# Kernel optimization log

Hardware: AMD Instinct MI355X
Metric: run time of the kernel (lower is better)

Reference implementation:

```python
import jax, jax.numpy as jnp
import numpy as np

N_NODES = 50000
N_EDGES = 640000
HID = 128
EDGE_FEAT = 4
NUM_G = 20
R_MIN, R_MAX = 0.0, 10.0

def setup_inputs() -> dict:
    key = jax.random.key(0)
    ks = jax.random.split(key, 16)
    s = lambda d: 1.0 / np.sqrt(d)
    return {
        'h': jax.random.normal(ks[0], (N_NODES, HID), jnp.float32),
        'x': jax.random.normal(ks[1], (N_NODES, 3), jnp.float32),
        'edge_index': jax.random.randint(ks[2], (2, N_EDGES), 0, N_NODES, dtype=jnp.int64),
        'mask_ligand': jnp.ones((N_NODES,), jnp.float32),
        'edge_attr': jax.random.normal(ks[3], (N_EDGES, EDGE_FEAT), jnp.float32),
        'We1': jax.random.normal(ks[4], (2*HID+EDGE_FEAT+NUM_G, HID), jnp.float32) * s(2*HID+EDGE_FEAT+NUM_G),
        'be1': jnp.zeros((HID,), jnp.float32),
        'We2': jax.random.normal(ks[5], (HID, HID), jnp.float32) * s(HID),
        'be2': jnp.zeros((HID,), jnp.float32),
        'Winf': jax.random.normal(ks[6], (HID, 1), jnp.float32) * s(HID),
        'binf': jnp.zeros((1,), jnp.float32),
        'Wx1': jax.random.normal(ks[7], (HID, HID), jnp.float32) * s(HID),
        'bx1': jnp.zeros((HID,), jnp.float32),
        'Wx2': jax.random.normal(ks[8], (HID, 1), jnp.float32) * 0.001 * s(HID),
        'Wn1': jax.random.normal(ks[9], (2*HID, HID), jnp.float32) * s(2*HID),
        'bn1': jnp.zeros((HID,), jnp.float32),
        'Wn2': jax.random.normal(ks[10], (HID, HID), jnp.float32) * s(HID),
        'bn2': jnp.zeros((HID,), jnp.float32),
    }

def reference(h, x, edge_index, mask_ligand, edge_attr,
              We1, be1, We2, be2, Winf, binf, Wx1, bx1, Wx2, Wn1, bn1, Wn2, bn2):
    n = h.shape[0]
    src, dst = edge_index[0], edge_index[1]
    hi, hj = h[dst], h[src]                      # [E, H] gathers
    rel_x = x[dst] - x[src]                      # [E, 3]
    d_sq = jnp.sum(rel_x**2, axis=-1, keepdims=True)  # [E, 1]
    d = jnp.sqrt(d_sq + 1e-8)
    # GaussianSmearing(r_min=0, r_max=10, num_gaussians=20)
    offset = jnp.linspace(R_MIN, R_MAX, NUM_G, dtype=h.dtype)
    coeff = -0.5 / (offset[1] - offset[0])**2
    d_feat = jnp.exp(coeff * (d - offset)**2)    # [E, 20]
    edge_feat = jnp.concatenate([d_feat, edge_attr], axis=-1)
    # edge MLP (2 layers, silu, act_last=True)
    z = jnp.concatenate([hi, hj, edge_feat], axis=-1)
    mij = jax.nn.silu(jax.nn.silu(z @ We1 + be1) @ We2 + be2)  # [E, H]
    eij = jax.nn.sigmoid(mij @ Winf + binf)      # [E, 1]
    mi = jax.ops.segment_sum(mij * eij, dst, num_segments=n)   # [N, H]
    # node MLP (2 layers, silu, no act on last)
    nz = jnp.concatenate([mi, h], axis=-1)
    h_out = h + (jax.nn.silu(nz @ Wn1 + bn1) @ Wn2 + bn2)
    # coordinate update
    xg = jnp.tanh(jax.nn.silu(mij @ Wx1 + bx1) @ Wx2)          # [E, 1]
    delta_x = jax.ops.segment_sum(rel_x / (d + 1.0) * xg, dst, num_segments=n)
    x_out = x + delta_x * mask_ligand[:, None]
    return h_out, x_out
```

## Files before the change

kernel.cpp:

```cpp
#include <hip/hip_runtime.h>
#include <math.h>

#define NN 50000
#define NE 640000
#define H 128
#define EPB 32
#define NPB 32
#define ZB 296
#define BB 136
#define KP1 288
#define NZB 264

typedef __attribute__((ext_vector_type(8))) unsigned short u16x8;
typedef __attribute__((ext_vector_type(8))) __bf16 bf16x8;
typedef __attribute__((ext_vector_type(2))) __bf16 bf16x2;
typedef __attribute__((ext_vector_type(4))) float f32x4;

__device__ __forceinline__ float silu_f(float v) {
    return v / (1.0f + __expf(-v));
}

__device__ __forceinline__ unsigned short f2bf(float f) {
    unsigned int u = __builtin_bit_cast(unsigned int, f);
    u += 0x7FFFu + ((u >> 16) & 1u);
    return (unsigned short)(u >> 16);
}

__device__ __forceinline__ float bf2f(unsigned short s) {
    unsigned int u = ((unsigned int)s) << 16;
    return __builtin_bit_cast(float, u);
}

__device__ __forceinline__ unsigned int pkbf(float lo, float hi) {
#if __has_builtin(__builtin_amdgcn_cvt_pk_bf16_f32)
    bf16x2 v = __builtin_amdgcn_cvt_pk_bf16_f32(lo, hi);
    unsigned int r; __builtin_memcpy(&r, &v, 4); return r;
#else
    return (unsigned int)f2bf(lo) | ((unsigned int)f2bf(hi) << 16);
#endif
}

__device__ __forceinline__ f32x4 mfma16(u16x8 a, u16x8 b, f32x4 c) {
    return __builtin_amdgcn_mfma_f32_16x16x32_bf16(
        __builtin_bit_cast(bf16x8, a), __builtin_bit_cast(bf16x8, b), c, 0, 0, 0);
}

template<int KT, int INSTR, bool SYNC_BEFORE_EPI>
__device__ __forceinline__ void layer_mfma(
    const unsigned short* __restrict__ inbuf,
    const unsigned short* __restrict__ wt,
    const float* __restrict__ bias,
    unsigned short* __restrict__ outbuf,
    int wv, int quad, int r16)
{
    f32x4 acc[2][2] = {};
    const int F = wv * 32;
    #pragma unroll
    for (int ks = 0; ks < KT / 32; ks++) {
        int ko = ks * 32 + quad * 8;
        u16x8 b0 = *(const u16x8*)(inbuf + r16 * INSTR + ko);
        u16x8 b1 = *(const u16x8*)(inbuf + (16 + r16) * INSTR + ko);
        u16x8 a0 = *(const u16x8*)(wt + (size_t)(F + r16) * KT + ko);
        u16x8 a1 = *(const u16x8*)(wt + (size_t)(F + 16 + r16) * KT + ko);
        acc[0][0] = mfma16(a0, b0, acc[0][0]);
        acc[0][1] = mfma16(a0, b1, acc[0][1]);
        acc[1][0] = mfma16(a1, b0, acc[1][0]);
        acc[1][1] = mfma16(a1, b1, acc[1][1]);
    }
    if (SYNC_BEFORE_EPI) __syncthreads();
    #pragma unroll
    for (int rt = 0; rt < 2; rt++) {
        int f0 = F + rt * 16 + quad * 4;
        float4 bv = *(const float4*)(bias + f0);
        #pragma unroll
        for (int ci = 0; ci < 2; ci++) {
            int e = ci * 16 + r16;
            float s0 = silu_f(acc[rt][ci][0] + bv.x);
            float s1 = silu_f(acc[rt][ci][1] + bv.y);
            float s2 = silu_f(acc[rt][ci][2] + bv.z);
            float s3 = silu_f(acc[rt][ci][3] + bv.w);
            uint2 p = { pkbf(s0, s1), pkbf(s2, s3) };
            *(uint2*)(outbuf + e * BB + f0) = p;
        }
    }
}

__global__ __launch_bounds__(256) void convert_weights(
    const float* __restrict__ We1, const float* __restrict__ We2,
    const float* __restrict__ Wx1, const float* __restrict__ Wn1,
    const float* __restrict__ Wn2,
    unsigned short* __restrict__ w1t, unsigned short* __restrict__ w2t,
    unsigned short* __restrict__ wx1t, unsigned short* __restrict__ wn1t,
    unsigned short* __restrict__ wn2t)
{
    int i = blockIdx.x * 256 + threadIdx.x;
    const int S1 = 128 * KP1;
    const int S2 = 128 * 128;
    const int S3 = 128 * 256;
    if (i < S1) {
        int n = i / KP1, k = i % KP1;
        w1t[i] = (k < 280) ? f2bf(We1[k * H + n]) : (unsigned short)0;
    } else if (i < S1 + S2) {
        int j = i - S1; int n = j / H, k = j % H;
        w2t[j] = f2bf(We2[k * H + n]);
    } else if (i < S1 + 2 * S2) {
        int j = i - S1 - S2; int n = j / H, k = j % H;
        wx1t[j] = f2bf(Wx1[k * H + n]);
    } else if (i < S1 + 2 * S2 + S3) {
        int j = i - S1 - 2 * S2; int n = j / 256, k = j % 256;
        wn1t[j] = f2bf(Wn1[k * H + n]);
    } else if (i < S1 + 3 * S2 + S3) {
        int j = i - S1 - 2 * S2 - S3; int n = j / H, k = j % H;
        wn2t[j] = f2bf(Wn2[k * H + n]);
    }
}

__global__ __launch_bounds__(256) void zero_kernel(float4* __restrict__ p, int n4) {
    int i = blockIdx.x * 256 + threadIdx.x;
    if (i < n4) p[i] = make_float4(0.f, 0.f, 0.f, 0.f);
}

__global__ __launch_bounds__(256, 5) void edge_kernel(
    const float* __restrict__ h, const float* __restrict__ x,
    const int* __restrict__ ei, const float* __restrict__ edge_attr,
    const unsigned short* __restrict__ w1t, const float* __restrict__ be1,
    const unsigned short* __restrict__ w2t, const float* __restrict__ be2,
    const float* __restrict__ Winf, const float* __restrict__ binf,
    const unsigned short* __restrict__ wx1t, const float* __restrict__ bx1,
    const float* __restrict__ Wx2,
    float* __restrict__ mi, float* __restrict__ dx)
{
    __shared__ unsigned short zs[EPB * ZB];
    __shared__ unsigned short m2[EPB * BB];
    __shared__ float relx_s[EPB][3];
    __shared__ float eij_s[EPB];
    __shared__ float epart[4][EPB];
    __shared__ float xpart[4][EPB];
    __shared__ int dst_s[EPB];
    __shared__ int src_s[EPB];
    __shared__ float winf_s[H];
    __shared__ float wx2_s[H];

    unsigned short* m1 = zs;

    const int t = threadIdx.x;
    const int e0 = blockIdx.x * EPB;

    if (t < EPB) {
        src_s[t] = ei[e0 + t];
        dst_s[t] = ei[NE + e0 + t];
    }
    if (t >= 128 && t < 256) {
        winf_s[t - 128] = Winf[t - 128];
        wx2_s[t - 128] = Wx2[t - 128];
    }
    __syncthreads();

    {
        int e = t >> 3, l = t & 7;
        int s = src_s[e], d = dst_s[e];
        const float4* hd = (const float4*)(h + (size_t)d * H);
        const float4* hs = (const float4*)(h + (size_t)s * H);
        unsigned short* zr = zs + e * ZB;
        float4 v0 = hd[l * 4 + 0], v1 = hd[l * 4 + 1];
        float4 v2 = hd[l * 4 + 2], v3 = hd[l * 4 + 3];
        uint4 p0 = { pkbf(v0.x, v0.y), pkbf(v0.z, v0.w), pkbf(v1.x, v1.y), pkbf(v1.z, v1.w) };
        uint4 p1 = { pkbf(v2.x, v2.y), pkbf(v2.z, v2.w), pkbf(v3.x, v3.y), pkbf(v3.z, v3.w) };
        *(uint4*)(zr + l * 16) = p0;
        *(uint4*)(zr + l * 16 + 8) = p1;
        float4 w0 = hs[l * 4 + 0], w1 = hs[l * 4 + 1];
        float4 w2 = hs[l * 4 + 2], w3 = hs[l * 4 + 3];
        uint4 q0 = { pkbf(w0.x, w0.y), pkbf(w0.z, w0.w), pkbf(w1.x, w1.y), pkbf(w1.z, w1.w) };
        uint4 q1 = { pkbf(w2.x, w2.y), pkbf(w2.z, w2.w), pkbf(w3.x, w3.y), pkbf(w3.z, w3.w) };
        *(uint4*)(zr + 128 + l * 16) = q0;
        *(uint4*)(zr + 128 + l * 16 + 8) = q1;
    }
    if (t < EPB) {
        int s = src_s[t], d = dst_s[t];
        float rx = x[d * 3 + 0] - x[s * 3 + 0];
        float ry = x[d * 3 + 1] - x[s * 3 + 1];
        float rz = x[d * 3 + 2] - x[s * 3 + 2];
        float d2 = rx * rx + ry * ry + rz * rz;
        float dd = sqrtf(d2 + 1e-8f);
        float inv = 1.0f / (dd + 1.0f);
        relx_s[t][0] = rx * inv;
        relx_s[t][1] = ry * inv;
        relx_s[t][2] = rz * inv;
        const float step = 10.0f / 19.0f;
        const float coeff = -0.5f / (step * step);
        unsigned short* zr = zs + t * ZB;
        #pragma unroll
        for (int g = 0; g < 20; g++) {
            float df = dd - step * (float)g;
            zr[256 + g] = f2bf(__expf(coeff * df * df));
        }
        #pragma unroll
        for (int j = 0; j < 4; j++)
            zr[276 + j] = f2bf(edge_attr[(size_t)(e0 + t) * 4 + j]);
        #pragma unroll
        for (int j = 280; j < ZB; j++) zr[j] = 0;
    }
    __syncthreads();

    const int wv = t >> 6, lane = t & 63;
    const int quad = lane >> 4, r16 = lane & 15;
    const int F = wv * 32;

    layer_mfma<KP1, ZB, true>(zs, w1t, be1, m1, wv, quad, r16);
    __syncthreads();

    {
        f32x4 acc[2][2] = {};
        #pragma unroll
        for (int ks = 0; ks < H / 32; ks++) {
            int ko = ks * 32 + quad * 8;
            u16x8 b0 = *(const u16x8*)(m1 + r16 * BB + ko);
            u16x8 b1 = *(const u16x8*)(m1 + (16 + r16) * BB + ko);
            u16x8 a0 = *(const u16x8*)(w2t + (size_t)(F + r16) * H + ko);
            u16x8 a1 = *(const u16x8*)(w2t + (size_t)(F + 16 + r16) * H + ko);
            acc[0][0] = mfma16(a0, b0, acc[0][0]);
            acc[0][1] = mfma16(a0, b1, acc[0][1]);
            acc[1][0] = mfma16(a1, b0, acc[1][0]);
            acc[1][1] = mfma16(a1, b1, acc[1][1]);
        }
        float ep[2] = {0.f, 0.f};
        #pragma unroll
        for (int rt = 0; rt < 2; rt++) {
            int f0 = F + rt * 16 + quad * 4;
            float4 bv = *(const float4*)(be2 + f0);
            float4 wf = *(const float4*)(winf_s + f0);
            #pragma unroll
            for (int ci = 0; ci < 2; ci++) {
                int e = ci * 16 + r16;
                float s0 = silu_f(acc[rt][ci][0] + bv.x);
                float s1 = silu_f(acc[rt][ci][1] + bv.y);
                float s2 = silu_f(acc[rt][ci][2] + bv.z);
                float s3 = silu_f(acc[rt][ci][3] + bv.w);
                ep[ci] += s0 * wf.x + s1 * wf.y + s2 * wf.z + s3 * wf.w;
                uint2 p = { pkbf(s0, s1), pkbf(s2, s3) };
                *(uint2*)(m2 + e * BB + f0) = p;
            }
        }
        #pragma unroll
        for (int ci = 0; ci < 2; ci++) {
            ep[ci] += __shfl_xor(ep[ci], 16, 64);
            ep[ci] += __shfl_xor(ep[ci], 32, 64);
        }
        if (quad == 0) {
            epart[wv][r16] = ep[0];
            epart[wv][16 + r16] = ep[1];
        }
    }
    __syncthreads();

    if (t < EPB) {
        float s = epart[0][t] + epart[1][t] + epart[2][t] + epart[3][t] + binf[0];
        eij_s[t] = 1.0f / (1.0f + __expf(-s));
    }

    {
        f32x4 acc[2][2] = {};
        #pragma unroll
        for (int ks = 0; ks < H / 32; ks++) {
            int ko = ks * 32 + quad * 8;
            u16x8 b0 = *(const u16x8*)(m2 + r16 * BB + ko);
            u16x8 b1 = *(const u16x8*)(m2 + (16 + r16) * BB + ko);
            u16x8 a0 = *(const u16x8*)(wx1t + (size_t)(F + r16) * H + ko);
            u16x8 a1 = *(const u16x8*)(wx1t + (size_t)(F + 16 + r16) * H + ko);
            acc[0][0] = mfma16(a0, b0, acc[0][0]);
            acc[0][1] = mfma16(a0, b1, acc[0][1]);
            acc[1][0] = mfma16(a1, b0, acc[1][0]);
            acc[1][1] = mfma16(a1, b1, acc[1][1]);
        }
        float xp[2] = {0.f, 0.f};
        #pragma unroll
        for (int rt = 0; rt < 2; rt++) {
            int f0 = F + rt * 16 + quad * 4;
            float4 bv = *(const float4*)(bx1 + f0);
            float4 wf = *(const float4*)(wx2_s + f0);
            #pragma unroll
            for (int ci = 0; ci < 2; ci++) {
                xp[ci] += silu_f(acc[rt][ci][0] + bv.x) * wf.x
                        + silu_f(acc[rt][ci][1] + bv.y) * wf.y
                        + silu_f(acc[rt][ci][2] + bv.z) * wf.z
                        + silu_f(acc[rt][ci][3] + bv.w) * wf.w;
            }
        }
        #pragma unroll
        for (int ci = 0; ci < 2; ci++) {
            xp[ci] += __shfl_xor(xp[ci], 16, 64);
            xp[ci] += __shfl_xor(xp[ci], 32, 64);
        }
        if (quad == 0) {
            xpart[wv][r16] = xp[0];
            xpart[wv][16 + r16] = xp[1];
        }
    }
    __syncthreads();

    {
        int k = t & 127, eh = t >> 7;
        for (int e = eh; e < EPB; e += 2) {
            float mv = bf2f(m2[e * BB + k]) * eij_s[e];
            atomicAdd(&mi[(size_t)dst_s[e] * H + k], mv);
        }
        if (t < EPB * 3) {
            int e = t / 3, dim = t % 3;
            float xs = xpart[0][e] + xpart[1][e] + xpart[2][e] + xpart[3][e];
            float xg = tanhf(xs);
            atomicAdd(&dx[(size_t)dst_s[e] * 3 + dim], relx_s[e][dim] * xg);
        }
    }
}

__global__ __launch_bounds__(256, 6) void node_kernel(
    const float* __restrict__ h, const float* __restrict__ x,
    const float* __restrict__ mask,
    const unsigned short* __restrict__ wn1t, const float* __restrict__ bn1,
    const unsigned short* __restrict__ wn2t, const float* __restrict__ bn2,
    float* __restrict__ mi_hout, float* __restrict__ dx_xout)
{
    __shared__ unsigned short nzs[NPB * NZB];
    __shared__ unsigned short nbuf[NPB * BB];

    const int t = threadIdx.x;
    const int n0 = blockIdx.x * NPB;

    {
        int r = t >> 3, l = t & 7;
        int n = n0 + r;
        unsigned short* zr = nzs + r * NZB;
        if (n < NN) {
            const float4* mi4 = (const float4*)(mi_hout + (size_t)n * H);
            const float4* h4  = (const float4*)(h + (size_t)n * H);
            float4 v0 = mi4[l * 4 + 0], v1 = mi4[l * 4 + 1];
            float4 v2 = mi4[l * 4 + 2], v3 = mi4[l * 4 + 3];
            uint4 p0 = { pkbf(v0.x, v0.y), pkbf(v0.z, v0.w), pkbf(v1.x, v1.y), pkbf(v1.z, v1.w) };
            uint4 p1 = { pkbf(v2.x, v2.y), pkbf(v2.z, v2.w), pkbf(v3.x, v3.y), pkbf(v3.z, v3.w) };
            *(uint4*)(zr + l * 16) = p0;
            *(uint4*)(zr + l * 16 + 8) = p1;
            float4 w0 = h4[l * 4 + 0], w1 = h4[l * 4 + 1];
            float4 w2 = h4[l * 4 + 2], w3 = h4[l * 4 + 3];
            uint4 q0 = { pkbf(w0.x, w0.y), pkbf(w0.z, w0.w), pkbf(w1.x, w1.y), pkbf(w1.z, w1.w) };
            uint4 q1 = { pkbf(w2.x, w2.y), pkbf(w2.z, w2.w), pkbf(w3.x, w3.y), pkbf(w3.z, w3.w) };
            *(uint4*)(zr + 128 + l * 16) = q0;
            *(uint4*)(zr + 128 + l * 16 + 8) = q1;
        } else {
            uint4 zf = {0u, 0u, 0u, 0u};
            *(uint4*)(zr + l * 16) = zf;
            *(uint4*)(zr + l * 16 + 8) = zf;
            *(uint4*)(zr + 128 + l * 16) = zf;
            *(uint4*)(zr + 128 + l * 16 + 8) = zf;
        }
    }

    float xo = 0.f;
    int xn = -1, xdim = 0;
    if (t < NPB * 3) {
        int r = t / 3; xdim = t % 3;
        int n = n0 + r;
        if (n < NN) {
            xn = n;
            xo = x[(size_t)n * 3 + xdim] + dx_xout[(size_t)n * 3 + xdim] * mask[n];
        }
    }
    __syncthreads();

    if (xn >= 0) dx_xout[(size_t)xn * 3 + xdim] = xo;

    const int wv = t >> 6, lane = t & 63;
    const int quad = lane >> 4, r16 = lane & 15;

    layer_mfma<2 * H, NZB, false>(nzs, wn1t, bn1, nbuf, wv, quad, r16);
    __syncthreads();

    {
        f32x4 acc[2][2] = {};
        const int F = wv * 32;
        #pragma unroll
        for (int ks = 0; ks < H / 32; ks++) {
            int ko = ks * 32 + quad * 8;
            u16x8 b0 = *(const u16x8*)(nbuf + r16 * BB + ko);
            u16x8 b1 = *(const u16x8*)(nbuf + (16 + r16) * BB + ko);
            u16x8 a0 = *(const u16x8*)(wn2t + (size_t)(F + r16) * H + ko);
            u16x8 a1 = *(const u16x8*)(wn2t + (size_t)(F + 16 + r16) * H + ko);
            acc[0][0] = mfma16(a0, b0, acc[0][0]);
            acc[0][1] = mfma16(a0, b1, acc[0][1]);
            acc[1][0] = mfma16(a1, b0, acc[1][0]);
            acc[1][1] = mfma16(a1, b1, acc[1][1]);
        }
        #pragma unroll
        for (int rt = 0; rt < 2; rt++) {
            int f0 = F + rt * 16 + quad * 4;
            float4 bv = *(const float4*)(bn2 + f0);
            #pragma unroll
            for (int ci = 0; ci < 2; ci++) {
                int n = n0 + ci * 16 + r16;
                if (n < NN) {
                    float4 hv = *(const float4*)(h + (size_t)n * H + f0);
                    float4 o;
                    o.x = hv.x + acc[rt][ci][0] + bv.x;
                    o.y = hv.y + acc[rt][ci][1] + bv.y;
                    o.z = hv.z + acc[rt][ci][2] + bv.z;
                    o.w = hv.w + acc[rt][ci][3] + bv.w;
                    *(float4*)(mi_hout + (size_t)n * H + f0) = o;
                }
            }
        }
    }
}

extern "C" void kernel_launch(void* const* d_in, const int* in_sizes, int n_in,
                              void* d_out, int out_size, void* d_ws, size_t ws_size,
                              hipStream_t stream) {
    const float* h     = (const float*)d_in[0];
    const float* x     = (const float*)d_in[1];
    const int*   ei    = (const int*)d_in[2];
    const float* mask  = (const float*)d_in[3];
    const float* eattr = (const float*)d_in[4];
    const float* We1   = (const float*)d_in[5];
    const float* be1   = (const float*)d_in[6];
    const float* We2   = (const float*)d_in[7];
    const float* be2   = (const float*)d_in[8];
    const float* Winf  = (const float*)d_in[9];
    const float* binf  = (const float*)d_in[10];
    const float* Wx1   = (const float*)d_in[11];
    const float* bx1   = (const float*)d_in[12];
    const float* Wx2   = (const float*)d_in[13];
    const float* Wn1   = (const float*)d_in[14];
    const float* bn1   = (const float*)d_in[15];
    const float* Wn2   = (const float*)d_in[16];
    const float* bn2   = (const float*)d_in[17];

    float* mi = (float*)d_out;
    float* dx = mi + (size_t)NN * H;

    unsigned short* w1t  = (unsigned short*)d_ws;
    unsigned short* w2t  = w1t + 128 * KP1;
    unsigned short* wx1t = w2t + 128 * H;
    unsigned short* wn1t = wx1t + 128 * H;
    unsigned short* wn2t = wn1t + 128 * 256;

    const int wconv_total = 128 * KP1 + 3 * 128 * H + 128 * 256;
    convert_weights<<<(wconv_total + 255) / 256, 256, 0, stream>>>(
        We1, We2, Wx1, Wn1, Wn2, w1t, w2t, wx1t, wn1t, wn2t);

    const int total4 = (NN * H + NN * 3) / 4;
    zero_kernel<<<(total4 + 255) / 256, 256, 0, stream>>>((float4*)d_out, total4);

    edge_kernel<<<NE / EPB, 256, 0, stream>>>(
        h, x, ei, eattr, w1t, be1, w2t, be2, Winf, binf, wx1t, bx1, Wx2, mi, dx);

    node_kernel<<<(NN + NPB - 1) / NPB, 256, 0, stream>>>(
        h, x, mask, wn1t, bn1, wn2t, bn2, mi, dx);
}
```

Baseline: 525.0 us.

## Alias LDS buffers, raise occupancy bounds, use fast reciprocal activations

```diff
diff --git a/kernel.cpp b/kernel.cpp
--- a/kernel.cpp
+++ b/kernel.cpp
@@ -16,8 +16,24 @@
 typedef __attribute__((ext_vector_type(2))) __bf16 bf16x2;
 typedef __attribute__((ext_vector_type(4))) float f32x4;
 
+__device__ __forceinline__ float frcp(float x) {
+#if __has_builtin(__builtin_amdgcn_rcpf)
+    return __builtin_amdgcn_rcpf(x);
+#else
+    return 1.0f / x;
+#endif
+}
+
 __device__ __forceinline__ float silu_f(float v) {
-    return v / (1.0f + __expf(-v));
+    return v * frcp(1.0f + __expf(-v));
+}
+
+__device__ __forceinline__ float sigmoid_f(float v) {
+    return frcp(1.0f + __expf(-v));
+}
+
+__device__ __forceinline__ float tanh_f(float v) {
+    return 1.0f - 2.0f * frcp(1.0f + __expf(2.0f * v));
 }
 
 __device__ __forceinline__ unsigned short f2bf(float f) {
@@ -120,7 +136,7 @@
     if (i < n4) p[i] = make_float4(0.f, 0.f, 0.f, 0.f);
 }
 
-__global__ __launch_bounds__(256, 5) void edge_kernel(
+__global__ __launch_bounds__(256, 7) void edge_kernel(
     const float* __restrict__ h, const float* __restrict__ x,
     const int* __restrict__ ei, const float* __restrict__ edge_attr,
     const unsigned short* __restrict__ w1t, const float* __restrict__ be1,
@@ -131,34 +147,28 @@
     float* __restrict__ mi, float* __restrict__ dx)
 {
     __shared__ unsigned short zs[EPB * ZB];
-    __shared__ unsigned short m2[EPB * BB];
     __shared__ float relx_s[EPB][3];
     __shared__ float eij_s[EPB];
     __shared__ float epart[4][EPB];
     __shared__ float xpart[4][EPB];
     __shared__ int dst_s[EPB];
-    __shared__ int src_s[EPB];
     __shared__ float winf_s[H];
     __shared__ float wx2_s[H];
 
     unsigned short* m1 = zs;
+    unsigned short* m2 = zs + EPB * BB;
 
     const int t = threadIdx.x;
     const int e0 = blockIdx.x * EPB;
 
-    if (t < EPB) {
-        src_s[t] = ei[e0 + t];
-        dst_s[t] = ei[NE + e0 + t];
-    }
     if (t >= 128 && t < 256) {
         winf_s[t - 128] = Winf[t - 128];
         wx2_s[t - 128] = Wx2[t - 128];
     }
-    __syncthreads();
 
     {
         int e = t >> 3, l = t & 7;
-        int s = src_s[e], d = dst_s[e];
+        int s = ei[e0 + e], d = ei[NE + e0 + e];
         const float4* hd = (const float4*)(h + (size_t)d * H);
         const float4* hs = (const float4*)(h + (size_t)s * H);
         unsigned short* zr = zs + e * ZB;
@@ -176,13 +186,14 @@
         *(uint4*)(zr + 128 + l * 16 + 8) = q1;
     }
     if (t < EPB) {
-        int s = src_s[t], d = dst_s[t];
+        int s = ei[e0 + t], d = ei[NE + e0 + t];
+        dst_s[t] = d;
         float rx = x[d * 3 + 0] - x[s * 3 + 0];
         float ry = x[d * 3 + 1] - x[s * 3 + 1];
         float rz = x[d * 3 + 2] - x[s * 3 + 2];
         float d2 = rx * rx + ry * ry + rz * rz;
         float dd = sqrtf(d2 + 1e-8f);
-        float inv = 1.0f / (dd + 1.0f);
+        float inv = frcp(dd + 1.0f);
         relx_s[t][0] = rx * inv;
         relx_s[t][1] = ry * inv;
         relx_s[t][2] = rz * inv;
@@ -255,7 +266,7 @@
 
     if (t < EPB) {
         float s = epart[0][t] + epart[1][t] + epart[2][t] + epart[3][t] + binf[0];
-        eij_s[t] = 1.0f / (1.0f + __expf(-s));
+        eij_s[t] = sigmoid_f(s);
     }
 
     {
@@ -307,13 +318,13 @@
         if (t < EPB * 3) {
             int e = t / 3, dim = t % 3;
             float xs = xpart[0][e] + xpart[1][e] + xpart[2][e] + xpart[3][e];
-            float xg = tanhf(xs);
+            float xg = tanh_f(xs);
             atomicAdd(&dx[(size_t)dst_s[e] * 3 + dim], relx_s[e][dim] * xg);
         }
     }
 }
 
-__global__ __launch_bounds__(256, 6) void node_kernel(
+__global__ __launch_bounds__(256, 8) void node_kernel(
     const float* __restrict__ h, const float* __restrict__ x,
     const float* __restrict__ mask,
     const unsigned short* __restrict__ wn1t, const float* __restrict__ bn1,
@@ -321,7 +332,8 @@
     float* __restrict__ mi_hout, float* __restrict__ dx_xout)
 {
     __shared__ unsigned short nzs[NPB * NZB];
-    __shared__ unsigned short nbuf[NPB * BB];
+
+    unsigned short* nbuf = nzs;
 
     const int t = threadIdx.x;
     const int n0 = blockIdx.x * NPB;
@@ -371,7 +383,7 @@
     const int wv = t >> 6, lane = t & 63;
     const int quad = lane >> 4, r16 = lane & 15;
 
-    layer_mfma<2 * H, NZB, false>(nzs, wn1t, bn1, nbuf, wv, quad, r16);
+    layer_mfma<2 * H, NZB, true>(nzs, wn1t, bn1, nbuf, wv, quad, r16);
     __syncthreads();
 
     {
```

Result: no change. 522.2 us (-0.5%).
